# Performance work log

Measured on AMD Instinct MI355X. Metric: run time of the kernel, lower is better.

## Reference

```python
import jax, jax.numpy as jnp
import numpy as np
from jax import lax

N, C, H, W = 4, 256, 64, 64
R = 2          # upsample ratio (scale_factor)
K = 5          # CARAFE up_kernel
COMP = 64      # CARAFEPack compressed_channels
EPS = 1e-5     # BatchNorm eps


def setup_inputs() -> dict:
    key = jax.random.key(0)
    ks = jax.random.split(key, 8)
    w = lambda k, s: jax.random.normal(k, s, jnp.float32) * 0.05
    return {
        "low_feature": jax.random.normal(ks[0], (N, C, H * R, W * R), jnp.float32),
        "high_feature": jax.random.normal(ks[1], (N, C, H, W), jnp.float32),
        "w_cc": w(ks[2], (COMP, C, 1, 1)),            # channel compressor 1x1
        "b_cc": jnp.zeros((COMP,), jnp.float32),
        "w_ce": w(ks[3], (K * K * R * R, COMP, 3, 3)), # content encoder 3x3
        "b_ce": jnp.zeros((K * K * R * R,), jnp.float32),
        "w_conv2": w(ks[4], (C, C, 1, 1)),
        "b_conv2": jnp.zeros((C,), jnp.float32),
        "w_bott": w(ks[5], (C, 2 * C, 1, 1)),          # bottleneck 1x1, no bias
        "gamma": jnp.ones((C,), jnp.float32),
        "beta": jnp.zeros((C,), jnp.float32),
    }


def _conv1x1(x, w, b=None):
    y = jnp.einsum('nchw,oc->nohw', x, w[:, :, 0, 0])
    if b is not None:
        y = y + b[None, :, None, None]
    return y


def _conv3x3(x, w, b):
    y = lax.conv_general_dilated(x, w, (1, 1), [(1, 1), (1, 1)],
                                 dimension_numbers=('NCHW', 'OIHW', 'NCHW'))
    return y + b[None, :, None, None]


def _pixel_shuffle(x, r):
    n, c, h, w = x.shape
    c2 = c // (r * r)
    x = x.reshape(n, c2, r, r, h, w).transpose(0, 1, 4, 2, 5, 3)
    return x.reshape(n, c2, h * r, w * r)


def _carafe(x, w_cc, b_cc, w_ce, b_ce):
    n, c, h, w = x.shape
    # predicted kernels: compress -> encode -> pixel_shuffle -> softmax over k^2
    mask = _conv3x3(_conv1x1(x, w_cc, b_cc), w_ce, b_ce)      # [N, K*K*R*R, H, W]
    mask = _pixel_shuffle(mask, R)                            # [N, K*K, H*R, W*R]
    mask = jax.nn.softmax(mask, axis=1)                       # group=1 -> over K*K
    # k x k neighborhoods of x (zero-padded), kernel index = ky*K + kx
    pad = K // 2
    xp = jnp.pad(x, ((0, 0), (0, 0), (pad, pad), (pad, pad)))
    patches = jnp.stack([xp[:, :, dy:dy + h, dx:dx + w]
                         for dy in range(K) for dx in range(K)], axis=2)  # [N,C,K*K,H,W]
    # each output pixel (i,j) reads source (i//R, j//R) neighborhood
    mr = mask.reshape(n, K * K, h, R, w, R)
    out = jnp.einsum('nckhw,nkhawb->nchawb', patches, mr)
    return out.reshape(n, c, h * R, w * R)


def reference(low_feature, high_feature, w_cc, b_cc, w_ce, b_ce,
              w_conv2, b_conv2, w_bott, gamma, beta):
    hf = _carafe(high_feature, w_cc, b_cc, w_ce, b_ce)        # [N,C,H*R,W*R]
    value = _conv1x1(hf, w_conv2, b_conv2)
    x = jnp.concatenate([value, hf], axis=1)                  # [N,2C,.,.]
    x = _conv1x1(x, w_bott)
    # BatchNorm (training-mode batch statistics) + ReLU
    mean = jnp.mean(x, axis=(0, 2, 3), keepdims=True)
    var = jnp.var(x, axis=(0, 2, 3), keepdims=True)
    x = (x - mean) * lax.rsqrt(var + EPS)
    x = x * gamma[None, :, None, None] + beta[None, :, None, None]
    return jax.nn.relu(x)
```

## Files before the change

### kernel.cpp

```cpp
#include <hip/hip_runtime.h>
#include <hip/hip_bf16.h>

#define N_    4
#define C_    256
#define PS_   4096
#define PO_   16384
#define COMP_ 64
#define QCH_  100
#define KK_   25

typedef unsigned short u16;
typedef __attribute__((ext_vector_type(8))) short short8;
typedef __attribute__((ext_vector_type(4))) float f32x4;

__device__ __forceinline__ u16 f2bu(float f) {
    __hip_bfloat16 h = __float2bfloat16(f);
    return __builtin_bit_cast(u16, h);
}

__global__ __launch_bounds__(256) void k_weff(const float* __restrict__ w_bott,
        const float* __restrict__ w_conv2, const float* __restrict__ b_conv2,
        u16* __restrict__ Weff_bf, float* __restrict__ beff) {
    int o = blockIdx.x, c = threadIdx.x;
    __shared__ float wb[512];
    wb[c]       = w_bott[o * 512 + c];
    wb[c + 256] = w_bott[o * 512 + 256 + c];
    __syncthreads();
    float acc = wb[256 + c];
    #pragma unroll 8
    for (int m = 0; m < 256; ++m)
        acc += wb[m] * w_conv2[m * 256 + c];
    Weff_bf[o * 256 + c] = f2bu(acc);
    if (c == 0) {
        float be = 0.f;
        for (int m = 0; m < 256; ++m) be += wb[m] * b_conv2[m];
        beff[o] = be;
    }
}

__global__ __launch_bounds__(256) void k_prep(const float* __restrict__ w_ce,
        const float* __restrict__ w_cc, u16* __restrict__ Wb, u16* __restrict__ Wcc_bf) {
    int bid = blockIdx.x;
    if (bid < 288) {
        int i = bid * 256 + threadIdx.x;
        int q = i / 576, u = i - q * 576;
        float v = (q < 100) ? w_ce[q * 576 + u] : 0.f;
        Wb[i] = f2bu(v);
    } else {
        int j = (bid - 288) * 256 + threadIdx.x;
        Wcc_bf[j] = f2bu(w_cc[j]);
    }
}

__global__ __launch_bounds__(256) void k_compress_mfma(const u16* __restrict__ Wcc_bf,
        const float* __restrict__ high, const float* __restrict__ b_cc,
        float* __restrict__ comp) {
    int tid = threadIdx.x;
    int wid = tid >> 6, lane = tid & 63;
    int col = lane & 15, quad = lane >> 4;
    int px0 = blockIdx.x * 128;
    int n = px0 >> 12, pxb = px0 & 4095;
    __shared__ u16 As[64 * 40];
    __shared__ u16 Bs[128 * 40];
    f32x4 acc[8] = {};
    #pragma unroll 1
    for (int k0 = 0; k0 < 256; k0 += 32) {
        __syncthreads();
        {
            int row = tid >> 2, seg = tid & 3;
            short8 av = *reinterpret_cast<const short8*>(Wcc_bf + row * 256 + k0 + seg * 8);
            *reinterpret_cast<short8*>(&As[row * 40 + seg * 8]) = av;
        }
        #pragma unroll
        for (int it = 0; it < 8; ++it) {
            int idx = it * 256 + tid;
            int c = (idx >> 7) * 2, px = idx & 127;
            const float* hp = high + (n * C_ + k0 + c) * PS_ + pxb + px;
            unsigned lo = f2bu(hp[0]);
            unsigned hi = f2bu(hp[PS_]);
            *reinterpret_cast<unsigned*>(&Bs[px * 40 + c]) = lo | (hi << 16);
        }
        __syncthreads();
        short8 a = *reinterpret_cast<const short8*>(&As[(wid * 16 + col) * 40 + quad * 8]);
        #pragma unroll
        for (int nt = 0; nt < 8; ++nt) {
            short8 b = *reinterpret_cast<const short8*>(&Bs[(nt * 16 + col) * 40 + quad * 8]);
            acc[nt] = __builtin_amdgcn_mfma_f32_16x16x32_bf16(a, b, acc[nt], 0, 0, 0);
        }
    }
    #pragma unroll
    for (int r = 0; r < 4; ++r) {
        int m = wid * 16 + quad * 4 + r;
        float bias = b_cc[m];
        float* cp = comp + (n * COMP_ + m) * PS_ + pxb + col;
        #pragma unroll
        for (int nt = 0; nt < 8; ++nt)
            cp[nt * 16] = acc[nt][r] + bias;
    }
}

__global__ __launch_bounds__(256) void k_im2col(const float* __restrict__ comp,
        u16* __restrict__ Icol) {
    int b = blockIdx.x;
    int n = b >> 6, tile = b & 63;
    int ty0 = (tile >> 3) << 3, tx0 = (tile & 7) << 3;
    int tid = threadIdx.x;
    __shared__ float ct[64 * 100];
    for (int idx = tid; idx < 6400; idx += 256) {
        int cc = idx / 100, r = idx - cc * 100;
        int yy = ty0 - 1 + r / 10, xx = tx0 - 1 + (r % 10);
        float v = 0.f;
        if ((unsigned)yy < 64u && (unsigned)xx < 64u)
            v = comp[(n * COMP_ + cc) * PS_ + yy * 64 + xx];
        ct[idx] = v;
    }
    __syncthreads();
    int u0 = tid * 2, u1 = u0 + 1;
    int c0 = (unsigned)u0 / 9u, t0 = u0 - c0 * 9;
    int c1 = (unsigned)u1 / 9u, t1 = u1 - c1 * 9;
    int off0 = c0 * 100 + (t0 / 3) * 10 + (t0 % 3);
    int off1 = c1 * 100 + (t1 / 3) * 10 + (t1 % 3);
    int u2 = 512 + tid * 2, u3 = u2 + 1;
    int c2 = (unsigned)u2 / 9u, t2 = u2 - c2 * 9;
    int c3 = (unsigned)u3 / 9u, t3 = u3 - c3 * 9;
    int off2 = c2 * 100 + (t2 / 3) * 10 + (t2 % 3);
    int off3 = c3 * 100 + (t3 / 3) * 10 + (t3 % 3);
    #pragma unroll 1
    for (int px = 0; px < 64; ++px) {
        int py = px >> 3, pxx = px & 7;
        int base = py * 10 + pxx;
        int gpx = n * PS_ + (ty0 + py) * 64 + tx0 + pxx;
        u16* dst = Icol + gpx * 576;
        unsigned lo = f2bu(ct[off0 + base]);
        unsigned hi = f2bu(ct[off1 + base]);
        *reinterpret_cast<unsigned*>(dst + u0) = lo | (hi << 16);
        if (tid < 32) {
            unsigned lo2 = f2bu(ct[off2 + base]);
            unsigned hi2 = f2bu(ct[off3 + base]);
            *reinterpret_cast<unsigned*>(dst + u2) = lo2 | (hi2 << 16);
        }
    }
}

__global__ __launch_bounds__(256) void k_encode_mfma(const u16* __restrict__ Wb,
        const u16* __restrict__ Icol, const float* __restrict__ b_ce,
        float* __restrict__ mask_raw) {
    int tid = threadIdx.x;
    int wid = tid >> 6, lane = tid & 63;
    int col = lane & 15, quad = lane >> 4;
    int px0 = blockIdx.x * 128;
    __shared__ u16 As[128 * 40];
    __shared__ u16 Bs[128 * 40];
    f32x4 acc[2][8] = {};
    #pragma unroll 1
    for (int k0 = 0; k0 < 576; k0 += 32) {
        __syncthreads();
        #pragma unroll
        for (int it = 0; it < 2; ++it) {
            int s = tid + it * 256;
            int row = s >> 2, seg = s & 3;
            short8 av = *reinterpret_cast<const short8*>(Wb + row * 576 + k0 + seg * 8);
            *reinterpret_cast<short8*>(&As[row * 40 + seg * 8]) = av;
            short8 bv = *reinterpret_cast<const short8*>(Icol + (px0 + row) * 576 + k0 + seg * 8);
            *reinterpret_cast<short8*>(&Bs[row * 40 + seg * 8]) = bv;
        }
        __syncthreads();
        short8 a0 = *reinterpret_cast<const short8*>(&As[(wid * 32 + col) * 40 + quad * 8]);
        short8 a1 = *reinterpret_cast<const short8*>(&As[(wid * 32 + 16 + col) * 40 + quad * 8]);
        #pragma unroll
        for (int nt = 0; nt < 8; ++nt) {
            short8 b = *reinterpret_cast<const short8*>(&Bs[(nt * 16 + col) * 40 + quad * 8]);
            acc[0][nt] = __builtin_amdgcn_mfma_f32_16x16x32_bf16(a0, b, acc[0][nt], 0, 0, 0);
            acc[1][nt] = __builtin_amdgcn_mfma_f32_16x16x32_bf16(a1, b, acc[1][nt], 0, 0, 0);
        }
    }
    int nimg = px0 >> 12;
    int pbase = px0 & 4095;
    #pragma unroll
    for (int mi = 0; mi < 2; ++mi) {
        int qbase = (wid * 2 + mi) * 16 + quad * 4;
        #pragma unroll
        for (int r = 0; r < 4; ++r) {
            int q = qbase + r;
            if (q < 100) {
                float bias = b_ce[q];
                float* mp = mask_raw + (nimg * QCH_ + q) * PS_ + pbase + col;
                #pragma unroll
                for (int nt = 0; nt < 8; ++nt)
                    mp[nt * 16] = acc[mi][nt][r] + bias;
            }
        }
    }
}

__global__ __launch_bounds__(256) void k_ygemm_mfma(const u16* __restrict__ Weff_bf,
        const float* __restrict__ high, float* __restrict__ Yt) {
    int tid = threadIdx.x;
    int wid = tid >> 6, lane = tid & 63;
    int col = lane & 15, quad = lane >> 4;
    int px0 = blockIdx.x * 128;
    int o0 = blockIdx.y * 128;
    int n = px0 >> 12, pxb = px0 & 4095;
    __shared__ u16 As[128 * 40];
    __shared__ u16 Bs[128 * 40];
    f32x4 acc[2][8] = {};
    #pragma unroll 1
    for (int k0 = 0; k0 < 256; k0 += 32) {
        __syncthreads();
        #pragma unroll
        for (int it = 0; it < 2; ++it) {
            int s = tid + it * 256;
            int row = s >> 2, seg = s & 3;
            short8 av = *reinterpret_cast<const short8*>(Weff_bf + (o0 + row) * 256 + k0 + seg * 8);
            *reinterpret_cast<short8*>(&As[row * 40 + seg * 8]) = av;
        }
        #pragma unroll
        for (int it = 0; it < 8; ++it) {
            int idx = it * 256 + tid;
            int c = (idx >> 7) * 2, px = idx & 127;
            const float* hp = high + (n * C_ + k0 + c) * PS_ + pxb + px;
            unsigned lo = f2bu(hp[0]);
            unsigned hi = f2bu(hp[PS_]);
            *reinterpret_cast<unsigned*>(&Bs[px * 40 + c]) = lo | (hi << 16);
        }
        __syncthreads();
        short8 a0 = *reinterpret_cast<const short8*>(&As[(wid * 32 + col) * 40 + quad * 8]);
        short8 a1 = *reinterpret_cast<const short8*>(&As[(wid * 32 + 16 + col) * 40 + quad * 8]);
        #pragma unroll
        for (int nt = 0; nt < 8; ++nt) {
            short8 b = *reinterpret_cast<const short8*>(&Bs[(nt * 16 + col) * 40 + quad * 8]);
            acc[0][nt] = __builtin_amdgcn_mfma_f32_16x16x32_bf16(a0, b, acc[0][nt], 0, 0, 0);
            acc[1][nt] = __builtin_amdgcn_mfma_f32_16x16x32_bf16(a1, b, acc[1][nt], 0, 0, 0);
        }
    }
    #pragma unroll
    for (int mi = 0; mi < 2; ++mi) {
        int ob = o0 + wid * 32 + mi * 16 + quad * 4;
        #pragma unroll
        for (int nt = 0; nt < 8; ++nt) {
            int gpx = px0 + nt * 16 + col;
            *reinterpret_cast<f32x4*>(Yt + gpx * 256 + ob) = acc[mi][nt];
        }
    }
}

__global__ __launch_bounds__(256) void k_carafe(const float* __restrict__ Yt,
        const float* __restrict__ mask_raw, const float* __restrict__ beff,
        float* __restrict__ xout) {
    int tile = blockIdx.x;
    int n = blockIdx.y;
    int half = blockIdx.z;
    int sh0 = (tile >> 3) << 3, sw0 = (tile & 7) << 3;
    int tid = threadIdx.x;
    int ty = tid >> 4, tx = tid & 15;
    int oi = sh0 * 2 + ty, oj = sw0 * 2 + tx;
    int h = sh0 + (ty >> 1), w = sw0 + (tx >> 1);
    int sub = ((ty & 1) << 1) | (tx & 1);
    float v[25];
    const float* mp = mask_raw + n * QCH_ * PS_ + h * 64 + w;
    #pragma unroll
    for (int k = 0; k < 25; ++k) v[k] = mp[(k * 4 + sub) * PS_];
    float mx = v[0];
    #pragma unroll
    for (int k = 1; k < 25; ++k) mx = fmaxf(mx, v[k]);
    float s = 0.f;
    #pragma unroll
    for (int k = 0; k < 25; ++k) { v[k] = __expf(v[k] - mx); s += v[k]; }
    float inv = 1.f / s;
    #pragma unroll
    for (int k = 0; k < 25; ++k) v[k] *= inv;

    __shared__ float xt[144 * 36];
    int sbase = ((ty >> 1) * 12 + (tx >> 1)) * 36;
    float* hp = xout + (n * C_ + half * 128) * PO_ + oi * 128 + oj;
    const float* Yb = Yt + (n * PS_) * 256 + half * 128;
    #pragma unroll 1
    for (int cg = 0; cg < 4; ++cg) {
        __syncthreads();
        #pragma unroll
        for (int it = 0; it < 18; ++it) {
            int idx = it * 256 + tid;
            int cc = idx & 31, sp = idx >> 5;
            int row = sp / 12, colm = sp - row * 12;
            int yy = sh0 - 2 + row, xx = sw0 - 2 + colm;
            float val = 0.f;
            if ((unsigned)yy < 64u && (unsigned)xx < 64u)
                val = Yb[(yy * 64 + xx) * 256 + cg * 32 + cc];
            xt[sp * 36 + cc] = val;
        }
        __syncthreads();
        #pragma unroll 1
        for (int c4 = 0; c4 < 8; ++c4) {
            int ch = half * 128 + cg * 32 + c4 * 4;
            float ax = beff[ch], ay = beff[ch + 1], az = beff[ch + 2], aw = beff[ch + 3];
            const float* base = xt + sbase + c4 * 4;
            #pragma unroll
            for (int ky = 0; ky < 5; ++ky) {
                #pragma unroll
                for (int kx = 0; kx < 5; ++kx) {
                    float4 yv = *reinterpret_cast<const float4*>(base + (ky * 12 + kx) * 36);
                    float m = v[ky * 5 + kx];
                    ax += m * yv.x; ay += m * yv.y; az += m * yv.z; aw += m * yv.w;
                }
            }
            int chl = cg * 32 + c4 * 4;
            hp[(chl + 0) * PO_] = ax;
            hp[(chl + 1) * PO_] = ay;
            hp[(chl + 2) * PO_] = az;
            hp[(chl + 3) * PO_] = aw;
        }
    }
}

__global__ __launch_bounds__(256) void k_stats(const float* __restrict__ xb,
        const float* __restrict__ gamma, const float* __restrict__ beta,
        float* __restrict__ scale, float* __restrict__ shift) {
    int o = blockIdx.x, tid = threadIdx.x;
    float s = 0.f, s2 = 0.f;
    for (int n = 0; n < 4; ++n) {
        const float* p = xb + (n * C_ + o) * PO_;
        #pragma unroll 4
        for (int i = 0; i < 64; ++i) {
            float v = p[i * 256 + tid];
            s += v; s2 += v * v;
        }
    }
    __shared__ float rs[256], rq[256];
    rs[tid] = s; rq[tid] = s2;
    __syncthreads();
    for (int off = 128; off > 0; off >>= 1) {
        if (tid < off) { rs[tid] += rs[tid + off]; rq[tid] += rq[tid + off]; }
        __syncthreads();
    }
    if (tid == 0) {
        float mean = rs[0] * (1.f / 65536.f);
        float var  = rq[0] * (1.f / 65536.f) - mean * mean;
        float sc = rsqrtf(var + 1e-5f) * gamma[o];
        scale[o] = sc;
        shift[o] = beta[o] - mean * sc;
    }
}

__global__ __launch_bounds__(256) void k_norm(float* __restrict__ xb,
        const float* __restrict__ scale, const float* __restrict__ shift) {
    int base = (blockIdx.x * 256 + threadIdx.x) * 4;
    int o = (base >> 14) & 255;
    float sc = scale[o], sh = shift[o];
    float4 v = *reinterpret_cast<const float4*>(xb + base);
    v.x = fmaxf(v.x * sc + sh, 0.f);
    v.y = fmaxf(v.y * sc + sh, 0.f);
    v.z = fmaxf(v.z * sc + sh, 0.f);
    v.w = fmaxf(v.w * sc + sh, 0.f);
    *reinterpret_cast<float4*>(xb + base) = v;
}

extern "C" void kernel_launch(void* const* d_in, const int* in_sizes, int n_in,
                              void* d_out, int out_size, void* d_ws, size_t ws_size,
                              hipStream_t stream) {
    const float* high    = (const float*)d_in[1];
    const float* w_cc    = (const float*)d_in[2];
    const float* b_cc    = (const float*)d_in[3];
    const float* w_ce    = (const float*)d_in[4];
    const float* b_ce    = (const float*)d_in[5];
    const float* w_conv2 = (const float*)d_in[6];
    const float* b_conv2 = (const float*)d_in[7];
    const float* w_bott  = (const float*)d_in[8];
    const float* gamma   = (const float*)d_in[9];
    const float* beta    = (const float*)d_in[10];

    char* ws = (char*)d_ws;
    float* beff    = (float*)(ws + 0);
    float* scale   = (float*)(ws + 1024);
    float* shift   = (float*)(ws + 2048);
    u16*   Weff_bf = (u16*)  (ws + 3072);
    u16*   Wcc_bf  = (u16*)  (ws + 134144);
    u16*   Wb      = (u16*)  (ws + 166912);
    float* mask    = (float*)(ws + 314368);
    float* comp    = (float*)(ws + 314368);
    u16*   Icol    = (u16*)  (ws + 6867968);
    float* Yt      = (float*)(ws + 6867968);
    float* xout    = (float*)d_out;

    k_weff         <<<256, 256, 0, stream>>>(w_bott, w_conv2, b_conv2, Weff_bf, beff);
    k_prep         <<<352, 256, 0, stream>>>(w_ce, w_cc, Wb, Wcc_bf);
    k_compress_mfma<<<128, 256, 0, stream>>>(Wcc_bf, high, b_cc, comp);
    k_im2col       <<<256, 256, 0, stream>>>(comp, Icol);
    k_encode_mfma  <<<128, 256, 0, stream>>>(Wb, Icol, b_ce, mask);
    k_ygemm_mfma   <<<dim3(128, 2), 256, 0, stream>>>(Weff_bf, high, Yt);
    k_carafe       <<<dim3(64, 4, 2), 256, 0, stream>>>(Yt, mask, beff, xout);
    k_stats        <<<256, 256, 0, stream>>>(xout, gamma, beta, scale, shift);
    k_norm         <<<16384, 256, 0, stream>>>(xout, scale, shift);
}
```

Before: 289.7 us.

## Merge prep kernels, halve GEMM pixel tiles, store Y in bf16, restructure CARAFE

The two weight-prep kernels are merged into one launch. The compress and encode GEMMs use 64-pixel tiles so twice as many blocks fill the GPU. The Y intermediate is stored as bf16, which halves its write and read traffic. The CARAFE kernel now has each thread handle one source pixel and all four sub-pixels, reusing each loaded neighbourhood value four times and staging the mask in shared memory. Costs include heavier register pressure in CARAFE (100 mask values held per thread) and extra bf16 rounding error in Y.

```diff
diff --git a/kernel.cpp b/kernel.cpp
--- a/kernel.cpp
+++ b/kernel.cpp
@@ -7,7 +7,6 @@
 #define PO_   16384
 #define COMP_ 64
 #define QCH_  100
-#define KK_   25
 
 typedef unsigned short u16;
 typedef __attribute__((ext_vector_type(8))) short short8;
@@ -17,37 +16,39 @@
     __hip_bfloat16 h = __float2bfloat16(f);
     return __builtin_bit_cast(u16, h);
 }
-
-__global__ __launch_bounds__(256) void k_weff(const float* __restrict__ w_bott,
+__device__ __forceinline__ float bits2f(unsigned u) {
+    union { unsigned i; float f; } v; v.i = u; return v.f;
+}
+
+__global__ __launch_bounds__(256) void k_prep(const float* __restrict__ w_bott,
         const float* __restrict__ w_conv2, const float* __restrict__ b_conv2,
-        u16* __restrict__ Weff_bf, float* __restrict__ beff) {
-    int o = blockIdx.x, c = threadIdx.x;
-    __shared__ float wb[512];
-    wb[c]       = w_bott[o * 512 + c];
-    wb[c + 256] = w_bott[o * 512 + 256 + c];
-    __syncthreads();
-    float acc = wb[256 + c];
-    #pragma unroll 8
-    for (int m = 0; m < 256; ++m)
-        acc += wb[m] * w_conv2[m * 256 + c];
-    Weff_bf[o * 256 + c] = f2bu(acc);
-    if (c == 0) {
-        float be = 0.f;
-        for (int m = 0; m < 256; ++m) be += wb[m] * b_conv2[m];
-        beff[o] = be;
-    }
-}
-
-__global__ __launch_bounds__(256) void k_prep(const float* __restrict__ w_ce,
-        const float* __restrict__ w_cc, u16* __restrict__ Wb, u16* __restrict__ Wcc_bf) {
+        const float* __restrict__ w_ce, const float* __restrict__ w_cc,
+        u16* __restrict__ Weff_bf, float* __restrict__ beff,
+        u16* __restrict__ Wb, u16* __restrict__ Wcc_bf) {
     int bid = blockIdx.x;
-    if (bid < 288) {
-        int i = bid * 256 + threadIdx.x;
+    if (bid < 256) {
+        int o = bid, c = threadIdx.x;
+        __shared__ float wb[512];
+        wb[c]       = w_bott[o * 512 + c];
+        wb[c + 256] = w_bott[o * 512 + 256 + c];
+        __syncthreads();
+        float acc = wb[256 + c];
+        #pragma unroll 8
+        for (int m = 0; m < 256; ++m)
+            acc += wb[m] * w_conv2[m * 256 + c];
+        Weff_bf[o * 256 + c] = f2bu(acc);
+        if (c == 0) {
+            float be = 0.f;
+            for (int m = 0; m < 256; ++m) be += wb[m] * b_conv2[m];
+            beff[o] = be;
+        }
+    } else if (bid < 544) {
+        int i = (bid - 256) * 256 + threadIdx.x;
         int q = i / 576, u = i - q * 576;
         float v = (q < 100) ? w_ce[q * 576 + u] : 0.f;
         Wb[i] = f2bu(v);
     } else {
-        int j = (bid - 288) * 256 + threadIdx.x;
+        int j = (bid - 544) * 256 + threadIdx.x;
         Wcc_bf[j] = f2bu(w_cc[j]);
     }
 }
@@ -58,11 +59,11 @@
     int tid = threadIdx.x;
     int wid = tid >> 6, lane = tid & 63;
     int col = lane & 15, quad = lane >> 4;
-    int px0 = blockIdx.x * 128;
+    int px0 = blockIdx.x * 64;
     int n = px0 >> 12, pxb = px0 & 4095;
     __shared__ u16 As[64 * 40];
-    __shared__ u16 Bs[128 * 40];
-    f32x4 acc[8] = {};
+    __shared__ u16 Bs[64 * 40];
+    f32x4 acc[4] = {};
     #pragma unroll 1
     for (int k0 = 0; k0 < 256; k0 += 32) {
         __syncthreads();
@@ -72,9 +73,9 @@
             *reinterpret_cast<short8*>(&As[row * 40 + seg * 8]) = av;
         }
         #pragma unroll
-        for (int it = 0; it < 8; ++it) {
+        for (int it = 0; it < 4; ++it) {
             int idx = it * 256 + tid;
-            int c = (idx >> 7) * 2, px = idx & 127;
+            int c = (idx >> 6) * 2, px = idx & 63;
             const float* hp = high + (n * C_ + k0 + c) * PS_ + pxb + px;
             unsigned lo = f2bu(hp[0]);
             unsigned hi = f2bu(hp[PS_]);
@@ -83,7 +84,7 @@
         __syncthreads();
         short8 a = *reinterpret_cast<const short8*>(&As[(wid * 16 + col) * 40 + quad * 8]);
         #pragma unroll
-        for (int nt = 0; nt < 8; ++nt) {
+        for (int nt = 0; nt < 4; ++nt) {
             short8 b = *reinterpret_cast<const short8*>(&Bs[(nt * 16 + col) * 40 + quad * 8]);
             acc[nt] = __builtin_amdgcn_mfma_f32_16x16x32_bf16(a, b, acc[nt], 0, 0, 0);
         }
@@ -94,7 +95,7 @@
         float bias = b_cc[m];
         float* cp = comp + (n * COMP_ + m) * PS_ + pxb + col;
         #pragma unroll
-        for (int nt = 0; nt < 8; ++nt)
+        for (int nt = 0; nt < 4; ++nt)
             cp[nt * 16] = acc[nt][r] + bias;
     }
 }
@@ -148,10 +149,11 @@
     int tid = threadIdx.x;
     int wid = tid >> 6, lane = tid & 63;
     int col = lane & 15, quad = lane >> 4;
-    int px0 = blockIdx.x * 128;
+    int px0 = blockIdx.x * 64;
+    int n = px0 >> 12, pxb = px0 & 4095;
     __shared__ u16 As[128 * 40];
-    __shared__ u16 Bs[128 * 40];
-    f32x4 acc[2][8] = {};
+    __shared__ u16 Bs[64 * 40];
+    f32x4 acc[2][4] = {};
     #pragma unroll 1
     for (int k0 = 0; k0 < 576; k0 += 32) {
         __syncthreads();
@@ -161,6 +163,9 @@
             int row = s >> 2, seg = s & 3;
             short8 av = *reinterpret_cast<const short8*>(Wb + row * 576 + k0 + seg * 8);
             *reinterpret_cast<short8*>(&As[row * 40 + seg * 8]) = av;
+        }
+        {
+            int row = tid >> 2, seg = tid & 3;
             short8 bv = *reinterpret_cast<const short8*>(Icol + (px0 + row) * 576 + k0 + seg * 8);
             *reinterpret_cast<short8*>(&Bs[row * 40 + seg * 8]) = bv;
         }
@@ -168,14 +173,12 @@
         short8 a0 = *reinterpret_cast<const short8*>(&As[(wid * 32 + col) * 40 + quad * 8]);
         short8 a1 = *reinterpret_cast<const short8*>(&As[(wid * 32 + 16 + col) * 40 + quad * 8]);
         #pragma unroll
-        for (int nt = 0; nt < 8; ++nt) {
+        for (int nt = 0; nt < 4; ++nt) {
             short8 b = *reinterpret_cast<const short8*>(&Bs[(nt * 16 + col) * 40 + quad * 8]);
             acc[0][nt] = __builtin_amdgcn_mfma_f32_16x16x32_bf16(a0, b, acc[0][nt], 0, 0, 0);
             acc[1][nt] = __builtin_amdgcn_mfma_f32_16x16x32_bf16(a1, b, acc[1][nt], 0, 0, 0);
         }
     }
-    int nimg = px0 >> 12;
-    int pbase = px0 & 4095;
     #pragma unroll
     for (int mi = 0; mi < 2; ++mi) {
         int qbase = (wid * 2 + mi) * 16 + quad * 4;
@@ -184,9 +187,9 @@
             int q = qbase + r;
             if (q < 100) {
                 float bias = b_ce[q];
-                float* mp = mask_raw + (nimg * QCH_ + q) * PS_ + pbase + col;
+                float* mp = mask_raw + (n * QCH_ + q) * PS_ + pxb + col;
                 #pragma unroll
-                for (int nt = 0; nt < 8; ++nt)
+                for (int nt = 0; nt < 4; ++nt)
                     mp[nt * 16] = acc[mi][nt][r] + bias;
             }
         }
@@ -194,7 +197,7 @@
 }
 
 __global__ __launch_bounds__(256) void k_ygemm_mfma(const u16* __restrict__ Weff_bf,
-        const float* __restrict__ high, float* __restrict__ Yt) {
+        const float* __restrict__ high, u16* __restrict__ Yt) {
     int tid = threadIdx.x;
     int wid = tid >> 6, lane = tid & 63;
     int col = lane & 15, quad = lane >> 4;
@@ -239,75 +242,102 @@
         #pragma unroll
         for (int nt = 0; nt < 8; ++nt) {
             int gpx = px0 + nt * 16 + col;
-            *reinterpret_cast<f32x4*>(Yt + gpx * 256 + ob) = acc[mi][nt];
-        }
-    }
-}
-
-__global__ __launch_bounds__(256) void k_carafe(const float* __restrict__ Yt,
+            unsigned lo = f2bu(acc[mi][nt][0]) | ((unsigned)f2bu(acc[mi][nt][1]) << 16);
+            unsigned hi = f2bu(acc[mi][nt][2]) | ((unsigned)f2bu(acc[mi][nt][3]) << 16);
+            uint2 pk; pk.x = lo; pk.y = hi;
+            *reinterpret_cast<uint2*>(Yt + (size_t)gpx * 256 + ob) = pk;
+        }
+    }
+}
+
+__global__ __launch_bounds__(256) void k_carafe(const u16* __restrict__ Yt,
         const float* __restrict__ mask_raw, const float* __restrict__ beff,
         float* __restrict__ xout) {
-    int tile = blockIdx.x;
-    int n = blockIdx.y;
-    int half = blockIdx.z;
+    int tile = blockIdx.x, n = blockIdx.y, half = blockIdx.z;
     int sh0 = (tile >> 3) << 3, sw0 = (tile & 7) << 3;
     int tid = threadIdx.x;
-    int ty = tid >> 4, tx = tid & 15;
-    int oi = sh0 * 2 + ty, oj = sw0 * 2 + tx;
-    int h = sh0 + (ty >> 1), w = sw0 + (tx >> 1);
-    int sub = ((ty & 1) << 1) | (tx & 1);
-    float v[25];
-    const float* mp = mask_raw + n * QCH_ * PS_ + h * 64 + w;
+    int px = tid & 63, g = tid >> 6;
+    int ly = px >> 3, lx = px & 7;
+    int h = sh0 + ly, w = sw0 + lx;
+
+    __shared__ float mt[6400];
+    __shared__ u16 xt[144 * 68];
+
+    for (int idx = tid; idx < 6400; idx += 256) {
+        int q = idx >> 6, p = idx & 63;
+        mt[idx] = mask_raw[(n * QCH_ + q) * PS_ + (sh0 + (p >> 3)) * 64 + sw0 + (p & 7)];
+    }
+    __syncthreads();
+
+    float vs[4][25];
     #pragma unroll
-    for (int k = 0; k < 25; ++k) v[k] = mp[(k * 4 + sub) * PS_];
-    float mx = v[0];
-    #pragma unroll
-    for (int k = 1; k < 25; ++k) mx = fmaxf(mx, v[k]);
-    float s = 0.f;
-    #pragma unroll
-    for (int k = 0; k < 25; ++k) { v[k] = __expf(v[k] - mx); s += v[k]; }
-    float inv = 1.f / s;
-    #pragma unroll
-    for (int k = 0; k < 25; ++k) v[k] *= inv;
-
-    __shared__ float xt[144 * 36];
-    int sbase = ((ty >> 1) * 12 + (tx >> 1)) * 36;
-    float* hp = xout + (n * C_ + half * 128) * PO_ + oi * 128 + oj;
-    const float* Yb = Yt + (n * PS_) * 256 + half * 128;
+    for (int s = 0; s < 4; ++s) {
+        #pragma unroll
+        for (int k = 0; k < 25; ++k) vs[s][k] = mt[(k * 4 + s) * 64 + px];
+        float mx = vs[s][0];
+        #pragma unroll
+        for (int k = 1; k < 25; ++k) mx = fmaxf(mx, vs[s][k]);
+        float sum = 0.f;
+        #pragma unroll
+        for (int k = 0; k < 25; ++k) { vs[s][k] = __expf(vs[s][k] - mx); sum += vs[s][k]; }
+        float inv = 1.f / sum;
+        #pragma unroll
+        for (int k = 0; k < 25; ++k) vs[s][k] *= inv;
+    }
+
+    const u16* Yb = Yt + (size_t)n * PS_ * 256;
+    float* hp_base = xout + (size_t)(n * C_) * PO_;
     #pragma unroll 1
-    for (int cg = 0; cg < 4; ++cg) {
-        __syncthreads();
-        #pragma unroll
-        for (int it = 0; it < 18; ++it) {
-            int idx = it * 256 + tid;
-            int cc = idx & 31, sp = idx >> 5;
+    for (int chunk = 0; chunk < 2; ++chunk) {
+        int ch0 = half * 128 + chunk * 64;
+        __syncthreads();
+        for (int idx = tid; idx < 1152; idx += 256) {
+            int sp = idx >> 3, seg = idx & 7;
             int row = sp / 12, colm = sp - row * 12;
             int yy = sh0 - 2 + row, xx = sw0 - 2 + colm;
-            float val = 0.f;
+            short8 val = {};
             if ((unsigned)yy < 64u && (unsigned)xx < 64u)
-                val = Yb[(yy * 64 + xx) * 256 + cg * 32 + cc];
-            xt[sp * 36 + cc] = val;
+                val = *reinterpret_cast<const short8*>(Yb + (size_t)(yy * 64 + xx) * 256 + ch0 + seg * 8);
+            *reinterpret_cast<short8*>(&xt[sp * 68 + seg * 8]) = val;
         }
         __syncthreads();
         #pragma unroll 1
-        for (int c4 = 0; c4 < 8; ++c4) {
-            int ch = half * 128 + cg * 32 + c4 * 4;
-            float ax = beff[ch], ay = beff[ch + 1], az = beff[ch + 2], aw = beff[ch + 3];
-            const float* base = xt + sbase + c4 * 4;
+        for (int cq = 0; cq < 4; ++cq) {
+            int c = g * 16 + cq * 4;
+            int ch = ch0 + c;
+            f32x4 bv = *reinterpret_cast<const f32x4*>(beff + ch);
+            float a_[4][4];
+            #pragma unroll
+            for (int s = 0; s < 4; ++s) {
+                a_[s][0] = bv[0]; a_[s][1] = bv[1]; a_[s][2] = bv[2]; a_[s][3] = bv[3];
+            }
+            const u16* bp = xt + (ly * 12 + lx) * 68 + c;
             #pragma unroll
             for (int ky = 0; ky < 5; ++ky) {
                 #pragma unroll
                 for (int kx = 0; kx < 5; ++kx) {
-                    float4 yv = *reinterpret_cast<const float4*>(base + (ky * 12 + kx) * 36);
-                    float m = v[ky * 5 + kx];
-                    ax += m * yv.x; ay += m * yv.y; az += m * yv.z; aw += m * yv.w;
+                    uint2 rv = *reinterpret_cast<const uint2*>(bp + (ky * 12 + kx) * 68);
+                    float f0 = bits2f(rv.x << 16);
+                    float f1 = bits2f(rv.x & 0xffff0000u);
+                    float f2 = bits2f(rv.y << 16);
+                    float f3 = bits2f(rv.y & 0xffff0000u);
+                    int k = ky * 5 + kx;
+                    #pragma unroll
+                    for (int s = 0; s < 4; ++s) {
+                        float m = vs[s][k];
+                        a_[s][0] += m * f0; a_[s][1] += m * f1;
+                        a_[s][2] += m * f2; a_[s][3] += m * f3;
+                    }
                 }
             }
-            int chl = cg * 32 + c4 * 4;
-            hp[(chl + 0) * PO_] = ax;
-            hp[(chl + 1) * PO_] = ay;
-            hp[(chl + 2) * PO_] = az;
-            hp[(chl + 3) * PO_] = aw;
+            #pragma unroll
+            for (int i = 0; i < 4; ++i) {
+                float* op = hp_base + (size_t)(ch + i) * PO_ + (2 * h) * 128 + 2 * w;
+                float2 r0; r0.x = a_[0][i]; r0.y = a_[1][i];
+                float2 r1; r1.x = a_[2][i]; r1.y = a_[3][i];
+                *reinterpret_cast<float2*>(op) = r0;
+                *reinterpret_cast<float2*>(op + 128) = r1;
+            }
         }
     }
 }
@@ -318,7 +348,7 @@
     int o = blockIdx.x, tid = threadIdx.x;
     float s = 0.f, s2 = 0.f;
     for (int n = 0; n < 4; ++n) {
-        const float* p = xb + (n * C_ + o) * PO_;
+        const float* p = xb + (size_t)(n * C_ + o) * PO_;
         #pragma unroll 4
         for (int i = 0; i < 64; ++i) {
             float v = p[i * 256 + tid];
@@ -378,14 +408,14 @@
     float* mask    = (float*)(ws + 314368);
     float* comp    = (float*)(ws + 314368);
     u16*   Icol    = (u16*)  (ws + 6867968);
-    float* Yt      = (float*)(ws + 6867968);
+    u16*   Yt      = (u16*)  (ws + 6867968);
     float* xout    = (float*)d_out;
 
-    k_weff         <<<256, 256, 0, stream>>>(w_bott, w_conv2, b_conv2, Weff_bf, beff);
-    k_prep         <<<352, 256, 0, stream>>>(w_ce, w_cc, Wb, Wcc_bf);
-    k_compress_mfma<<<128, 256, 0, stream>>>(Wcc_bf, high, b_cc, comp);
+    k_prep         <<<608, 256, 0, stream>>>(w_bott, w_conv2, b_conv2, w_ce, w_cc,
+                                             Weff_bf, beff, Wb, Wcc_bf);
+    k_compress_mfma<<<256, 256, 0, stream>>>(Wcc_bf, high, b_cc, comp);
     k_im2col       <<<256, 256, 0, stream>>>(comp, Icol);
-    k_encode_mfma  <<<128, 256, 0, stream>>>(Wb, Icol, b_ce, mask);
+    k_encode_mfma  <<<256, 256, 0, stream>>>(Wb, Icol, b_ce, mask);
     k_ygemm_mfma   <<<dim3(128, 2), 256, 0, stream>>>(Weff_bf, high, Yt);
     k_carafe       <<<dim3(64, 4, 2), 256, 0, stream>>>(Yt, mask, beff, xout);
     k_stats        <<<256, 256, 0, stream>>>(xout, gamma, beta, scale, shift);
```

Measured after the change: 272.1 us. 6.1% less time.
